# Kernel optimization log

Hardware: AMD Instinct MI355X
Metric: run time of the kernel (lower is better)

Reference implementation:

```python
import jax, jax.numpy as jnp
from jax import lax
import numpy as np

WS = 5  # window_size
H = 6   # hidden_size
IN = 3 * WS  # 15
OUT = 2


def setup_inputs() -> dict:
    key = jax.random.key(0)
    k1, k2, k3, k4, k5 = jax.random.split(key, 5)
    B, T = 8192, 1024
    one_full_traj = jax.random.normal(k1, (B, T, 3), dtype=jnp.float32)
    # nn.Linear-style params: y = x @ W.T + b
    W1 = jax.random.normal(k2, (H, IN), dtype=jnp.float32) * (1.0 / np.sqrt(IN))
    b1 = jax.random.normal(k3, (H,), dtype=jnp.float32) * 0.05
    W2 = jax.random.normal(k4, (OUT, H), dtype=jnp.float32) * (1.0 / np.sqrt(H))
    b2 = jax.random.normal(k5, (OUT,), dtype=jnp.float32) * 0.05
    return {"one_full_traj": one_full_traj, "W1": W1, "b1": b1, "W2": W2, "b2": b2}


def reference(one_full_traj, W1, b1, W2, b2):
    ws = WS
    B, T, _ = one_full_traj.shape

    def mlp(x):  # [B, 3*ws] -> [B, 2]
        return jnp.tanh(x @ W1.T + b1) @ W2.T + b2

    def make_inp(seq):  # [B, ws, 3] -> [B, 3*ws], channel-major per original cat order
        return jnp.transpose(seq, (0, 2, 1)).reshape(B, 3 * ws)

    # step 0
    out = mlp(make_inp(one_full_traj[:, :ws, :]))[:, None, :]  # [B, 1, 2]

    # warm-up loop t = 1 .. ws-1 (small fixed Python loop, matches original indexing)
    for t in range(1, ws):
        n = out.shape[1]  # == t
        tmp = jnp.concatenate(
            [one_full_traj[:, ws + (t - 1):ws + (t - 1) + n, 0:1], out], axis=2
        )  # [B, t, 3]
        seq = jnp.concatenate([one_full_traj[:, t:ws, :], tmp], axis=1)  # [B, ws, 3]
        out = jnp.concatenate([out, mlp(make_inp(seq))[:, None, :]], axis=1)

    # sliding window of the last ws predictions as carry.
    u = one_full_traj[:, :, 0]  # control channel, [B, T]

    def step(win, t):
        uw = lax.dynamic_slice_in_dim(u, t, ws, axis=1)  # [B, ws]
        seq = jnp.concatenate([uw[:, :, None], win], axis=2)  # [B, ws, 3]
        pred = mlp(make_inp(seq))  # [B, 2]
        win = jnp.concatenate([win[:, 1:, :], pred[:, None, :]], axis=1)
        return win, pred

    ts = jnp.arange(ws, T - ws)
    _, preds = lax.scan(step, out, ts)  # preds: [T-2*ws, B, 2]
    return jnp.concatenate([out, jnp.transpose(preds, (1, 0, 2))], axis=1)  # [B, T-ws, 2]
```

## Files before the change

### kernel.cpp

```cpp
#include <hip/hip_runtime.h>
#include <math.h>

#define TLEN  1024
#define NSTEP 1019

template <int CTRL>
__device__ __forceinline__ float dpp_add(float v) {
    union { int i; float f; } in, out;
    in.f = v;
    out.i = __builtin_amdgcn_update_dpp(0, in.i, CTRL, 0xF, 0xF, false);
    return v + out.f;
}
__device__ __forceinline__ float sum8(float v) {
    v = dpp_add<0xB1>(v);
    v = dpp_add<0x4E>(v);
    v = dpp_add<0x141>(v);
    return v;
}

__device__ __forceinline__ float fast_exp2(float z) {
#if __has_builtin(__builtin_amdgcn_exp2f)
    return __builtin_amdgcn_exp2f(z);
#else
    return exp2f(z);
#endif
}

__global__ __launch_bounds__(64) void MLP_or_nextstep_kernel(
    const float* __restrict__ traj,
    const float* __restrict__ W1,
    const float* __restrict__ b1,
    const float* __restrict__ W2,
    const float* __restrict__ b2,
    float* __restrict__ out)
{
    __shared__ float lds_u[TLEN][8];

    const int lane = threadIdx.x;
    const int g    = lane >> 3;
    const int n    = lane & 7;
    const int bstart = blockIdx.x * 8;
    const int b = bstart + g;

    const float* __restrict__ base = traj + (size_t)b * (TLEN * 3);
    float2* outb = (float2*)out + (size_t)b * NSTEP;
    const bool is_store_lane = (n == 0);

    {
        const int s_elem = lane & 7;
        const int s_row  = lane >> 3;
        const float* __restrict__ sbase = traj + (size_t)(bstart + s_elem) * (TLEN * 3);
        for (int j = 0; j < TLEN / 8; ++j) {
            const float* gp = sbase + (size_t)(8 * j + s_row) * 3;
            __builtin_amdgcn_global_load_lds(
                (const __attribute__((address_space(1))) void*)gp,
                (__attribute__((address_space(3))) void*)&lds_u[8 * j][0],
                4, 0, 0);
        }
    }

    const float KK = 2.8853900817779268f;
    const int nr = (n < 6) ? n : 5;
    float w1row[15], b1r;
#pragma unroll
    for (int j = 0; j < 15; ++j) w1row[j] = KK * W1[nr * 15 + j];
    b1r = KK * b1[nr];
    const float w2a_l = (n < 6) ? W2[n]     : 0.0f;
    const float w2b_l = (n < 6) ? W2[6 + n] : 0.0f;
    const float bias_a = (n == 6) ? b2[0] : 0.0f;
    const float bias_b = (n == 7) ? b2[1] : 0.0f;
    const float c1a = -2.0f * w2a_l, c0a = w2a_l + bias_a;
    const float c1b = -2.0f * w2b_l, c0b = w2b_l + bias_b;

    auto mlp = [&](const float* __restrict__ x, float& ya, float& yb) {
        float z0 = w1row[0] * x[0];
        float z1 = w1row[5] * x[5];
        float z2 = fmaf(w1row[10], x[10], b1r);
#pragma unroll
        for (int j = 1; j < 5; ++j) {
            z0 = fmaf(w1row[j],      x[j],      z0);
            z1 = fmaf(w1row[5 + j],  x[5 + j],  z1);
            z2 = fmaf(w1row[10 + j], x[10 + j], z2);
        }
        float z = (z0 + z1) + z2;
        float r = __builtin_amdgcn_rcpf(fast_exp2(z) + 1.0f);
        ya = sum8(fmaf(c1a, r, c0a));
        yb = sum8(fmaf(c1b, r, c0b));
    };

    float uu[12], vv[5], wc[5];
#pragma unroll
    for (int i = 0; i < 12; ++i) uu[i] = base[i * 3];
#pragma unroll
    for (int i = 0; i < 5; ++i) { vv[i] = base[i * 3 + 1]; wc[i] = base[i * 3 + 2]; }

    float pa[5], pb[5];
    {
        float x[15] = {uu[0],uu[1],uu[2],uu[3],uu[4],
                       vv[0],vv[1],vv[2],vv[3],vv[4],
                       wc[0],wc[1],wc[2],wc[3],wc[4]};
        mlp(x, pa[0], pb[0]);
    }
    {
        float x[15] = {uu[1],uu[2],uu[3],uu[4],uu[5],
                       vv[1],vv[2],vv[3],vv[4],pa[0],
                       wc[1],wc[2],wc[3],wc[4],pb[0]};
        mlp(x, pa[1], pb[1]);
    }
    {
        float x[15] = {uu[2],uu[3],uu[4],uu[6],uu[7],
                       vv[2],vv[3],vv[4],pa[0],pa[1],
                       wc[2],wc[3],wc[4],pb[0],pb[1]};
        mlp(x, pa[2], pb[2]);
    }
    {
        float x[15] = {uu[3],uu[4],uu[7],uu[8],uu[9],
                       vv[3],vv[4],pa[0],pa[1],pa[2],
                       wc[3],wc[4],pb[0],pb[1],pb[2]};
        mlp(x, pa[3], pb[3]);
    }
    {
        float x[15] = {uu[4],uu[8],uu[9],uu[10],uu[11],
                       vv[4],pa[0],pa[1],pa[2],pa[3],
                       wc[4],pb[0],pb[1],pb[2],pb[3]};
        mlp(x, pa[4], pb[4]);
    }
    if (is_store_lane) {
#pragma unroll
        for (int i = 0; i < 5; ++i) outb[i] = make_float2(pa[i], pb[i]);
    }

    __syncthreads();

    float aw[5], bw[5];
#pragma unroll
    for (int i = 0; i < 5; ++i) { aw[i] = pa[i]; bw[i] = pb[i]; }

    const float* up  = &lds_u[5][g];
    const float* upn;
    float2* sp = outb + n + 5;
    float unA[9], unB[9];

#pragma unroll
    for (int i = 0; i < 9; ++i) unA[i] = up[8 * i];
    upn = up + 40;

#define LOADN(BUF)                                                           \
    {                                                                        \
        _Pragma("unroll")                                                    \
        for (int i = 0; i < 9; ++i) BUF[i] = upn[8 * i];                     \
        upn += 40;                                                           \
    }

#define STEP(S, UN, J, M)                                                    \
    {                                                                        \
        float z0 = w1row[0] * UN[S];                                         \
        float z1 = w1row[5] * aw[(S) % 5];                                   \
        float z2 = fmaf(w1row[10], bw[(S) % 5], b1r);                        \
        z0 = fmaf(w1row[1], UN[(S) + 1], z0);                                \
        z1 = fmaf(w1row[6], aw[((S) + 1) % 5], z1);                          \
        z2 = fmaf(w1row[11], bw[((S) + 1) % 5], z2);                         \
        z0 = fmaf(w1row[2], UN[(S) + 2], z0);                                \
        z1 = fmaf(w1row[7], aw[((S) + 2) % 5], z1);                          \
        z2 = fmaf(w1row[12], bw[((S) + 2) % 5], z2);                         \
        z0 = fmaf(w1row[3], UN[(S) + 3], z0);                                \
        z1 = fmaf(w1row[8], aw[((S) + 3) % 5], z1);                          \
        z2 = fmaf(w1row[13], bw[((S) + 3) % 5], z2);                         \
        z0 = fmaf(w1row[4], UN[(S) + 4], z0);                                \
        z1 = fmaf(w1row[9], aw[((S) + 4) % 5], z1);                          \
        z2 = fmaf(w1row[14], bw[((S) + 4) % 5], z2);                         \
        float z = (z0 + z1) + z2;                                            \
        float r = __builtin_amdgcn_rcpf(fast_exp2(z) + 1.0f);                \
        float ya = sum8(fmaf(c1a, r, c0a));                                  \
        float yb = sum8(fmaf(c1b, r, c0b));                                  \
        if (n == (J)) { ka##M = ya; kb##M = yb; }                            \
        aw[(S) % 5] = ya; bw[(S) % 5] = yb;                                  \
    }

#define STORE(M) sp[8 * (M)] = make_float2(ka##M, kb##M);

    for (int sb = 0; sb < 25; ++sb) {
        float ka0 = 0, kb0 = 0, ka1 = 0, kb1 = 0, ka2 = 0, kb2 = 0,
              ka3 = 0, kb3 = 0, ka4 = 0, kb4 = 0;
        LOADN(unB)
        STEP(0, unA, 0, 0) STEP(1, unA, 1, 0) STEP(2, unA, 2, 0)
        STEP(3, unA, 3, 0) STEP(4, unA, 4, 0)
        LOADN(unA)
        STEP(0, unB, 5, 0) STEP(1, unB, 6, 0) STEP(2, unB, 7, 0) STORE(0)
        STEP(3, unB, 0, 1) STEP(4, unB, 1, 1)
        LOADN(unB)
        STEP(0, unA, 2, 1) STEP(1, unA, 3, 1) STEP(2, unA, 4, 1)
        STEP(3, unA, 5, 1) STEP(4, unA, 6, 1)
        LOADN(unA)
        STEP(0, unB, 7, 1) STORE(1)
        STEP(1, unB, 0, 2) STEP(2, unB, 1, 2) STEP(3, unB, 2, 2) STEP(4, unB, 3, 2)
        LOADN(unB)
        STEP(0, unA, 4, 2) STEP(1, unA, 5, 2) STEP(2, unA, 6, 2)
        STEP(3, unA, 7, 2) STORE(2)
        STEP(4, unA, 0, 3)
        LOADN(unA)
        STEP(0, unB, 1, 3) STEP(1, unB, 2, 3) STEP(2, unB, 3, 3)
        STEP(3, unB, 4, 3) STEP(4, unB, 5, 3)
        LOADN(unB)
        STEP(0, unA, 6, 3) STEP(1, unA, 7, 3) STORE(3)
        STEP(2, unA, 0, 4) STEP(3, unA, 1, 4) STEP(4, unA, 2, 4)
        LOADN(unA)
        STEP(0, unB, 3, 4) STEP(1, unB, 4, 4) STEP(2, unB, 5, 4)
        STEP(3, unB, 6, 4) STEP(4, unB, 7, 4) STORE(4)

        sp += 40;
    }

    float2* tp = outb + 1005;
#define TSTEP(S, UN, K)                                                      \
    {                                                                        \
        float z0 = w1row[0] * UN[S];                                         \
        float z1 = w1row[5] * aw[(S) % 5];                                   \
        float z2 = fmaf(w1row[10], bw[(S) % 5], b1r);                        \
        z0 = fmaf(w1row[1], UN[(S) + 1], z0);                                \
        z1 = fmaf(w1row[6], aw[((S) + 1) % 5], z1);                          \
        z2 = fmaf(w1row[11], bw[((S) + 1) % 5], z2);                         \
        z0 = fmaf(w1row[2], UN[(S) + 2], z0);                                \
        z1 = fmaf(w1row[7], aw[((S) + 2) % 5], z1);                          \
        z2 = fmaf(w1row[12], bw[((S) + 2) % 5], z2);                         \
        z0 = fmaf(w1row[3], UN[(S) + 3], z0);                                \
        z1 = fmaf(w1row[8], aw[((S) + 3) % 5], z1);                          \
        z2 = fmaf(w1row[13], bw[((S) + 3) % 5], z2);                         \
        z0 = fmaf(w1row[4], UN[(S) + 4], z0);                                \
        z1 = fmaf(w1row[9], aw[((S) + 4) % 5], z1);                          \
        z2 = fmaf(w1row[14], bw[((S) + 4) % 5], z2);                         \
        float z = (z0 + z1) + z2;                                            \
        float r = __builtin_amdgcn_rcpf(fast_exp2(z) + 1.0f);                \
        float ya = sum8(fmaf(c1a, r, c0a));                                  \
        float yb = sum8(fmaf(c1b, r, c0b));                                  \
        if (is_store_lane) tp[K] = make_float2(ya, yb);                      \
        aw[(S) % 5] = ya; bw[(S) % 5] = yb;                                  \
    }

    TSTEP(0, unA, 0) TSTEP(1, unA, 1) TSTEP(2, unA, 2) TSTEP(3, unA, 3) TSTEP(4, unA, 4)
    LOADN(unB)
    TSTEP(0, unB, 5) TSTEP(1, unB, 6) TSTEP(2, unB, 7) TSTEP(3, unB, 8) TSTEP(4, unB, 9)
    LOADN(unA)
    TSTEP(0, unA, 10) TSTEP(1, unA, 11) TSTEP(2, unA, 12) TSTEP(3, unA, 13)

#undef TSTEP
#undef STORE
#undef STEP
#undef LOADN
}

extern "C" void kernel_launch(void* const* d_in, const int* in_sizes, int n_in,
                              void* d_out, int out_size, void* d_ws, size_t ws_size,
                              hipStream_t stream) {
    const float* traj = (const float*)d_in[0];
    const float* W1   = (const float*)d_in[1];
    const float* b1   = (const float*)d_in[2];
    const float* W2   = (const float*)d_in[3];
    const float* b2   = (const float*)d_in[4];
    float* out = (float*)d_out;

    const int grid = 8192 / 8;
    MLP_or_nextstep_kernel<<<grid, 64, 0, stream>>>(traj, W1, b1, W2, b2, out);
}
```

Baseline: 246.7 us.

## Shorten the recurrence critical path by precomputing partial pre-activation sums one step ahead

Splits each step's hidden pre-activation into an input-only part and a window part. The input-only part is computed one block of five steps ahead and held in ping-pong register arrays. The window part, minus the newest prediction, is accumulated during the current step's exp/rcp latency. This leaves only two FMAs, an add, exp, rcp and the DPP reductions on the serial dependency chain between steps. The cost is extra registers, and the u-values are prefetched one block further ahead, so LDS reads go further past the last used element.

```diff
diff --git a/kernel.cpp b/kernel.cpp
--- a/kernel.cpp
+++ b/kernel.cpp
@@ -152,29 +152,59 @@
         upn += 40;                                                           \
     }
 
-#define STEP(S, UN, J, M)                                                    \
+    float duC[5], duD[5];
+#pragma unroll
+    for (int i = 0; i < 5; ++i) {
+        float d = w1row[0] * unA[i];
+        d = fmaf(w1row[1], unA[i + 1], d);
+        d = fmaf(w1row[2], unA[i + 2], d);
+        d = fmaf(w1row[3], unA[i + 3], d);
+        d = fmaf(w1row[4], unA[i + 4], d);
+        duC[i] = d;
+    }
+
+    LOADN(unB)
+
+    float pAc, pBc, pAn, pBn;
+    pAc = w1row[5] * aw[0];
+    pAc = fmaf(w1row[6], aw[1], pAc);
+    pAc = fmaf(w1row[7], aw[2], pAc);
+    pAc = fmaf(w1row[8], aw[3], pAc);
+    pBc = fmaf(w1row[10], bw[0], b1r);
+    pBc = fmaf(w1row[11], bw[1], pBc);
+    pBc = fmaf(w1row[12], bw[2], pBc);
+    pBc = fmaf(w1row[13], bw[3], pBc);
+
+#define STEP(S, DUC, DUN, UN, J, M)                                          \
     {                                                                        \
-        float z0 = w1row[0] * UN[S];                                         \
-        float z1 = w1row[5] * aw[(S) % 5];                                   \
-        float z2 = fmaf(w1row[10], bw[(S) % 5], b1r);                        \
-        z0 = fmaf(w1row[1], UN[(S) + 1], z0);                                \
-        z1 = fmaf(w1row[6], aw[((S) + 1) % 5], z1);                          \
-        z2 = fmaf(w1row[11], bw[((S) + 1) % 5], z2);                         \
-        z0 = fmaf(w1row[2], UN[(S) + 2], z0);                                \
-        z1 = fmaf(w1row[7], aw[((S) + 2) % 5], z1);                          \
-        z2 = fmaf(w1row[12], bw[((S) + 2) % 5], z2);                         \
-        z0 = fmaf(w1row[3], UN[(S) + 3], z0);                                \
-        z1 = fmaf(w1row[8], aw[((S) + 3) % 5], z1);                          \
-        z2 = fmaf(w1row[13], bw[((S) + 3) % 5], z2);                         \
-        z0 = fmaf(w1row[4], UN[(S) + 4], z0);                                \
-        z1 = fmaf(w1row[9], aw[((S) + 4) % 5], z1);                          \
-        z2 = fmaf(w1row[14], bw[((S) + 4) % 5], z2);                         \
-        float z = (z0 + z1) + z2;                                            \
-        float r = __builtin_amdgcn_rcpf(fast_exp2(z) + 1.0f);                \
+        float tA = fmaf(w1row[9],  aw[((S) + 4) % 5], pAc);                  \
+        float tB = fmaf(w1row[14], bw[((S) + 4) % 5], pBc);                  \
+        float z  = (DUC[S] + tA) + tB;                                       \
+        float e  = fast_exp2(z);                                             \
+             \
+        pAn = w1row[5] * aw[((S) + 1) % 5];                                  \
+        pAn = fmaf(w1row[6], aw[((S) + 2) % 5], pAn);                        \
+        pAn = fmaf(w1row[7], aw[((S) + 3) % 5], pAn);                        \
+        pAn = fmaf(w1row[8], aw[((S) + 4) % 5], pAn);                        \
+        pBn = fmaf(w1row[10], bw[((S) + 1) % 5], b1r);                       \
+        pBn = fmaf(w1row[11], bw[((S) + 2) % 5], pBn);                       \
+        pBn = fmaf(w1row[12], bw[((S) + 3) % 5], pBn);                       \
+        pBn = fmaf(w1row[13], bw[((S) + 4) % 5], pBn);                       \
+        {                                                                    \
+            float d = w1row[0] * UN[S];                                      \
+            d = fmaf(w1row[1], UN[(S) + 1], d);                              \
+            d = fmaf(w1row[2], UN[(S) + 2], d);                              \
+            d = fmaf(w1row[3], UN[(S) + 3], d);                              \
+            d = fmaf(w1row[4], UN[(S) + 4], d);                              \
+            DUN[S] = d;                                                      \
+        }                                                                    \
+                                        \
+        float r  = __builtin_amdgcn_rcpf(e + 1.0f);                          \
         float ya = sum8(fmaf(c1a, r, c0a));                                  \
         float yb = sum8(fmaf(c1b, r, c0b));                                  \
         if (n == (J)) { ka##M = ya; kb##M = yb; }                            \
         aw[(S) % 5] = ya; bw[(S) % 5] = yb;                                  \
+        pAc = pAn; pBc = pBn;                                                \
     }
 
 #define STORE(M) sp[8 * (M)] = make_float2(ka##M, kb##M);
@@ -182,31 +212,31 @@
     for (int sb = 0; sb < 25; ++sb) {
         float ka0 = 0, kb0 = 0, ka1 = 0, kb1 = 0, ka2 = 0, kb2 = 0,
               ka3 = 0, kb3 = 0, ka4 = 0, kb4 = 0;
-        LOADN(unB)
-        STEP(0, unA, 0, 0) STEP(1, unA, 1, 0) STEP(2, unA, 2, 0)
-        STEP(3, unA, 3, 0) STEP(4, unA, 4, 0)
-        LOADN(unA)
-        STEP(0, unB, 5, 0) STEP(1, unB, 6, 0) STEP(2, unB, 7, 0) STORE(0)
-        STEP(3, unB, 0, 1) STEP(4, unB, 1, 1)
-        LOADN(unB)
-        STEP(0, unA, 2, 1) STEP(1, unA, 3, 1) STEP(2, unA, 4, 1)
-        STEP(3, unA, 5, 1) STEP(4, unA, 6, 1)
-        LOADN(unA)
-        STEP(0, unB, 7, 1) STORE(1)
-        STEP(1, unB, 0, 2) STEP(2, unB, 1, 2) STEP(3, unB, 2, 2) STEP(4, unB, 3, 2)
-        LOADN(unB)
-        STEP(0, unA, 4, 2) STEP(1, unA, 5, 2) STEP(2, unA, 6, 2)
-        STEP(3, unA, 7, 2) STORE(2)
-        STEP(4, unA, 0, 3)
-        LOADN(unA)
-        STEP(0, unB, 1, 3) STEP(1, unB, 2, 3) STEP(2, unB, 3, 3)
-        STEP(3, unB, 4, 3) STEP(4, unB, 5, 3)
-        LOADN(unB)
-        STEP(0, unA, 6, 3) STEP(1, unA, 7, 3) STORE(3)
-        STEP(2, unA, 0, 4) STEP(3, unA, 1, 4) STEP(4, unA, 2, 4)
-        LOADN(unA)
-        STEP(0, unB, 3, 4) STEP(1, unB, 4, 4) STEP(2, unB, 5, 4)
-        STEP(3, unB, 6, 4) STEP(4, unB, 7, 4) STORE(4)
+        LOADN(unA)
+        STEP(0, duC, duD, unB, 0, 0) STEP(1, duC, duD, unB, 1, 0) STEP(2, duC, duD, unB, 2, 0)
+        STEP(3, duC, duD, unB, 3, 0) STEP(4, duC, duD, unB, 4, 0)
+        LOADN(unB)
+        STEP(0, duD, duC, unA, 5, 0) STEP(1, duD, duC, unA, 6, 0) STEP(2, duD, duC, unA, 7, 0) STORE(0)
+        STEP(3, duD, duC, unA, 0, 1) STEP(4, duD, duC, unA, 1, 1)
+        LOADN(unA)
+        STEP(0, duC, duD, unB, 2, 1) STEP(1, duC, duD, unB, 3, 1) STEP(2, duC, duD, unB, 4, 1)
+        STEP(3, duC, duD, unB, 5, 1) STEP(4, duC, duD, unB, 6, 1)
+        LOADN(unB)
+        STEP(0, duD, duC, unA, 7, 1) STORE(1)
+        STEP(1, duD, duC, unA, 0, 2) STEP(2, duD, duC, unA, 1, 2) STEP(3, duD, duC, unA, 2, 2) STEP(4, duD, duC, unA, 3, 2)
+        LOADN(unA)
+        STEP(0, duC, duD, unB, 4, 2) STEP(1, duC, duD, unB, 5, 2) STEP(2, duC, duD, unB, 6, 2)
+        STEP(3, duC, duD, unB, 7, 2) STORE(2)
+        STEP(4, duC, duD, unB, 0, 3)
+        LOADN(unB)
+        STEP(0, duD, duC, unA, 1, 3) STEP(1, duD, duC, unA, 2, 3) STEP(2, duD, duC, unA, 3, 3)
+        STEP(3, duD, duC, unA, 4, 3) STEP(4, duD, duC, unA, 5, 3)
+        LOADN(unA)
+        STEP(0, duC, duD, unB, 6, 3) STEP(1, duC, duD, unB, 7, 3) STORE(3)
+        STEP(2, duC, duD, unB, 0, 4) STEP(3, duC, duD, unB, 1, 4) STEP(4, duC, duD, unB, 2, 4)
+        LOADN(unB)
+        STEP(0, duD, duC, unA, 3, 4) STEP(1, duD, duC, unA, 4, 4) STEP(2, duD, duC, unA, 5, 4)
+        STEP(3, duD, duC, unA, 6, 4) STEP(4, duD, duC, unA, 7, 4) STORE(4)
 
         sp += 40;
     }
@@ -238,9 +268,8 @@
     }
 
     TSTEP(0, unA, 0) TSTEP(1, unA, 1) TSTEP(2, unA, 2) TSTEP(3, unA, 3) TSTEP(4, unA, 4)
-    LOADN(unB)
+    LOADN(unA)
     TSTEP(0, unB, 5) TSTEP(1, unB, 6) TSTEP(2, unB, 7) TSTEP(3, unB, 8) TSTEP(4, unB, 9)
-    LOADN(unA)
     TSTEP(0, unA, 10) TSTEP(1, unA, 11) TSTEP(2, unA, 12) TSTEP(3, unA, 13)
 
 #undef TSTEP
```

New measurement: 238.7 us. 1.03x faster.

## Interleave two independent trajectories per lane and precompute off-critical-path partial sums

Applied to the files above, without the earlier changes.

Each wave now handles 16 batch rows instead of 8, processing two independent recurrences (X and Y) interleaved per lane so their dependent exp/rcp/DPP chains can hide each other's latency. The control-input contribution and the first four terms of the feedback dot products are precomputed one step ahead, which shortens the serial dependency chain per step. The DPP reductions are batched four at a time. In exchange, register pressure roughly doubles, LDS use doubles, and the grid halves to 512 workgroups, which may underfill the GPU's compute units.

```diff
diff --git a/kernel.cpp b/kernel.cpp
--- a/kernel.cpp
+++ b/kernel.cpp
@@ -16,6 +16,11 @@
     v = dpp_add<0x4E>(v);
     v = dpp_add<0x141>(v);
     return v;
+}
+__device__ __forceinline__ void sum8x4(float& a, float& b, float& c, float& d) {
+    a = dpp_add<0xB1>(a);  b = dpp_add<0xB1>(b);  c = dpp_add<0xB1>(c);  d = dpp_add<0xB1>(d);
+    a = dpp_add<0x4E>(a);  b = dpp_add<0x4E>(b);  c = dpp_add<0x4E>(c);  d = dpp_add<0x4E>(d);
+    a = dpp_add<0x141>(a); b = dpp_add<0x141>(b); c = dpp_add<0x141>(c); d = dpp_add<0x141>(d);
 }
 
 __device__ __forceinline__ float fast_exp2(float z) {
@@ -34,27 +39,30 @@
     const float* __restrict__ b2,
     float* __restrict__ out)
 {
-    __shared__ float lds_u[TLEN][8];
+    __shared__ float lds_u[TLEN][16];
 
     const int lane = threadIdx.x;
     const int g    = lane >> 3;
     const int n    = lane & 7;
-    const int bstart = blockIdx.x * 8;
-    const int b = bstart + g;
-
-    const float* __restrict__ base = traj + (size_t)b * (TLEN * 3);
-    float2* outb = (float2*)out + (size_t)b * NSTEP;
+    const int bstart = blockIdx.x * 16;
+    const int bX = bstart + g;
+    const int bY = bstart + 8 + g;
+
+    const float* __restrict__ baseX = traj + (size_t)bX * (TLEN * 3);
+    const float* __restrict__ baseY = traj + (size_t)bY * (TLEN * 3);
+    float2* outbX = (float2*)out + (size_t)bX * NSTEP;
+    float2* outbY = (float2*)out + (size_t)bY * NSTEP;
     const bool is_store_lane = (n == 0);
 
     {
-        const int s_elem = lane & 7;
-        const int s_row  = lane >> 3;
+        const int s_elem = lane & 15;
+        const int s_row  = lane >> 4;
         const float* __restrict__ sbase = traj + (size_t)(bstart + s_elem) * (TLEN * 3);
-        for (int j = 0; j < TLEN / 8; ++j) {
-            const float* gp = sbase + (size_t)(8 * j + s_row) * 3;
+        for (int j = 0; j < TLEN / 4; ++j) {
+            const float* gp = sbase + (size_t)(4 * j + s_row) * 3;
             __builtin_amdgcn_global_load_lds(
                 (const __attribute__((address_space(1))) void*)gp,
-                (__attribute__((address_space(3))) void*)&lds_u[8 * j][0],
+                (__attribute__((address_space(3))) void*)&lds_u[4 * j][0],
                 4, 0, 0);
         }
     }
@@ -88,165 +96,272 @@
         yb = sum8(fmaf(c1b, r, c0b));
     };
 
-    float uu[12], vv[5], wc[5];
-#pragma unroll
-    for (int i = 0; i < 12; ++i) uu[i] = base[i * 3];
-#pragma unroll
-    for (int i = 0; i < 5; ++i) { vv[i] = base[i * 3 + 1]; wc[i] = base[i * 3 + 2]; }
-
-    float pa[5], pb[5];
-    {
-        float x[15] = {uu[0],uu[1],uu[2],uu[3],uu[4],
-                       vv[0],vv[1],vv[2],vv[3],vv[4],
-                       wc[0],wc[1],wc[2],wc[3],wc[4]};
-        mlp(x, pa[0], pb[0]);
-    }
-    {
-        float x[15] = {uu[1],uu[2],uu[3],uu[4],uu[5],
-                       vv[1],vv[2],vv[3],vv[4],pa[0],
-                       wc[1],wc[2],wc[3],wc[4],pb[0]};
-        mlp(x, pa[1], pb[1]);
-    }
-    {
-        float x[15] = {uu[2],uu[3],uu[4],uu[6],uu[7],
-                       vv[2],vv[3],vv[4],pa[0],pa[1],
-                       wc[2],wc[3],wc[4],pb[0],pb[1]};
-        mlp(x, pa[2], pb[2]);
-    }
-    {
-        float x[15] = {uu[3],uu[4],uu[7],uu[8],uu[9],
-                       vv[3],vv[4],pa[0],pa[1],pa[2],
-                       wc[3],wc[4],pb[0],pb[1],pb[2]};
-        mlp(x, pa[3], pb[3]);
-    }
-    {
-        float x[15] = {uu[4],uu[8],uu[9],uu[10],uu[11],
-                       vv[4],pa[0],pa[1],pa[2],pa[3],
-                       wc[4],pb[0],pb[1],pb[2],pb[3]};
-        mlp(x, pa[4], pb[4]);
-    }
-    if (is_store_lane) {
-#pragma unroll
-        for (int i = 0; i < 5; ++i) outb[i] = make_float2(pa[i], pb[i]);
-    }
+    float paX[5], pbX[5], paY[5], pbY[5];
+
+#define WARMUP(SFX)                                                              \
+    {                                                                            \
+        float uu[12], vv[5], wc[5];                                              \
+        _Pragma("unroll")                                                        \
+        for (int i = 0; i < 12; ++i) uu[i] = base##SFX[i * 3];                   \
+        _Pragma("unroll")                                                        \
+        for (int i = 0; i < 5; ++i) { vv[i] = base##SFX[i * 3 + 1];              \
+                                      wc[i] = base##SFX[i * 3 + 2]; }            \
+        {                                                                        \
+            float x[15] = {uu[0],uu[1],uu[2],uu[3],uu[4],                        \
+                           vv[0],vv[1],vv[2],vv[3],vv[4],                        \
+                           wc[0],wc[1],wc[2],wc[3],wc[4]};                       \
+            mlp(x, pa##SFX[0], pb##SFX[0]);                                      \
+        }                                                                        \
+        {                                                                        \
+            float x[15] = {uu[1],uu[2],uu[3],uu[4],uu[5],                        \
+                           vv[1],vv[2],vv[3],vv[4],pa##SFX[0],                   \
+                           wc[1],wc[2],wc[3],wc[4],pb##SFX[0]};                  \
+            mlp(x, pa##SFX[1], pb##SFX[1]);                                      \
+        }                                                                        \
+        {                                                                        \
+            float x[15] = {uu[2],uu[3],uu[4],uu[6],uu[7],                        \
+                           vv[2],vv[3],vv[4],pa##SFX[0],pa##SFX[1],              \
+                           wc[2],wc[3],wc[4],pb##SFX[0],pb##SFX[1]};             \
+            mlp(x, pa##SFX[2], pb##SFX[2]);                                      \
+        }                                                                        \
+        {                                                                        \
+            float x[15] = {uu[3],uu[4],uu[7],uu[8],uu[9],                        \
+                           vv[3],vv[4],pa##SFX[0],pa##SFX[1],pa##SFX[2],         \
+                           wc[3],wc[4],pb##SFX[0],pb##SFX[1],pb##SFX[2]};        \
+            mlp(x, pa##SFX[3], pb##SFX[3]);                                      \
+        }                                                                        \
+        {                                                                        \
+            float x[15] = {uu[4],uu[8],uu[9],uu[10],uu[11],                      \
+                           vv[4],pa##SFX[0],pa##SFX[1],pa##SFX[2],pa##SFX[3],    \
+                           wc[4],pb##SFX[0],pb##SFX[1],pb##SFX[2],pb##SFX[3]};   \
+            mlp(x, pa##SFX[4], pb##SFX[4]);                                      \
+        }                                                                        \
+        if (is_store_lane) {                                                     \
+            _Pragma("unroll")                                                    \
+            for (int i = 0; i < 5; ++i)                                          \
+                outb##SFX[i] = make_float2(pa##SFX[i], pb##SFX[i]);              \
+        }                                                                        \
+    }
+
+    WARMUP(X)
+    WARMUP(Y)
+#undef WARMUP
 
     __syncthreads();
 
-    float aw[5], bw[5];
-#pragma unroll
-    for (int i = 0; i < 5; ++i) { aw[i] = pa[i]; bw[i] = pb[i]; }
-
-    const float* up  = &lds_u[5][g];
-    const float* upn;
-    float2* sp = outb + n + 5;
-    float unA[9], unB[9];
-
-#pragma unroll
-    for (int i = 0; i < 9; ++i) unA[i] = up[8 * i];
-    upn = up + 40;
-
-#define LOADN(BUF)                                                           \
+    float awX[5], bwX[5], awY[5], bwY[5];
+#pragma unroll
+    for (int i = 0; i < 5; ++i) { awX[i] = paX[i]; bwX[i] = pbX[i];
+                                  awY[i] = paY[i]; bwY[i] = pbY[i]; }
+
+    const float* upX = &lds_u[5][g];
+    const float* upY = &lds_u[5][8 + g];
+    float2* spX = outbX + n + 5;
+    float2* spY = outbY + n + 5;
+    float unAX[9], unBX[9], unAY[9], unBY[9];
+
+#pragma unroll
+    for (int i = 0; i < 9; ++i) { unAX[i] = upX[16 * i]; unAY[i] = upY[16 * i]; }
+    const float* upnX = upX + 80;
+    const float* upnY = upY + 80;
+
+#define LOADN2(UB)                                                           \
     {                                                                        \
         _Pragma("unroll")                                                    \
-        for (int i = 0; i < 9; ++i) BUF[i] = upn[8 * i];                     \
-        upn += 40;                                                           \
-    }
-
-#define STEP(S, UN, J, M)                                                    \
+        for (int i = 0; i < 9; ++i) { un##UB##X[i] = upnX[16 * i];           \
+                                      un##UB##Y[i] = upnY[16 * i]; }         \
+        upnX += 80; upnY += 80;                                              \
+    }
+
+    float duCX[5], duDX[5], duCY[5], duDY[5];
+#pragma unroll
+    for (int i = 0; i < 5; ++i) {
+        float dX = w1row[0] * unAX[i];
+        float dY = w1row[0] * unAY[i];
+        dX = fmaf(w1row[1], unAX[i + 1], dX);
+        dY = fmaf(w1row[1], unAY[i + 1], dY);
+        dX = fmaf(w1row[2], unAX[i + 2], dX);
+        dY = fmaf(w1row[2], unAY[i + 2], dY);
+        dX = fmaf(w1row[3], unAX[i + 3], dX);
+        dY = fmaf(w1row[3], unAY[i + 3], dY);
+        dX = fmaf(w1row[4], unAX[i + 4], dX);
+        dY = fmaf(w1row[4], unAY[i + 4], dY);
+        duCX[i] = dX;
+        duCY[i] = dY;
+    }
+
+    LOADN2(B)
+
+    float pAcX, pBcX, pAnX, pBnX, pAcY, pBcY, pAnY, pBnY;
+    pAcX = w1row[5] * awX[0];
+    pAcY = w1row[5] * awY[0];
+    pAcX = fmaf(w1row[6], awX[1], pAcX);
+    pAcY = fmaf(w1row[6], awY[1], pAcY);
+    pAcX = fmaf(w1row[7], awX[2], pAcX);
+    pAcY = fmaf(w1row[7], awY[2], pAcY);
+    pAcX = fmaf(w1row[8], awX[3], pAcX);
+    pAcY = fmaf(w1row[8], awY[3], pAcY);
+    pBcX = fmaf(w1row[10], bwX[0], b1r);
+    pBcY = fmaf(w1row[10], bwY[0], b1r);
+    pBcX = fmaf(w1row[11], bwX[1], pBcX);
+    pBcY = fmaf(w1row[11], bwY[1], pBcY);
+    pBcX = fmaf(w1row[12], bwX[2], pBcX);
+    pBcY = fmaf(w1row[12], bwY[2], pBcY);
+    pBcX = fmaf(w1row[13], bwX[3], pBcX);
+    pBcY = fmaf(w1row[13], bwY[3], pBcY);
+
+#define STEP2(S, DC, DN, UB, J, M)                                           \
     {                                                                        \
-        float z0 = w1row[0] * UN[S];                                         \
-        float z1 = w1row[5] * aw[(S) % 5];                                   \
-        float z2 = fmaf(w1row[10], bw[(S) % 5], b1r);                        \
-        z0 = fmaf(w1row[1], UN[(S) + 1], z0);                                \
-        z1 = fmaf(w1row[6], aw[((S) + 1) % 5], z1);                          \
-        z2 = fmaf(w1row[11], bw[((S) + 1) % 5], z2);                         \
-        z0 = fmaf(w1row[2], UN[(S) + 2], z0);                                \
-        z1 = fmaf(w1row[7], aw[((S) + 2) % 5], z1);                          \
-        z2 = fmaf(w1row[12], bw[((S) + 2) % 5], z2);                         \
-        z0 = fmaf(w1row[3], UN[(S) + 3], z0);                                \
-        z1 = fmaf(w1row[8], aw[((S) + 3) % 5], z1);                          \
-        z2 = fmaf(w1row[13], bw[((S) + 3) % 5], z2);                         \
-        z0 = fmaf(w1row[4], UN[(S) + 4], z0);                                \
-        z1 = fmaf(w1row[9], aw[((S) + 4) % 5], z1);                          \
-        z2 = fmaf(w1row[14], bw[((S) + 4) % 5], z2);                         \
-        float z = (z0 + z1) + z2;                                            \
-        float r = __builtin_amdgcn_rcpf(fast_exp2(z) + 1.0f);                \
-        float ya = sum8(fmaf(c1a, r, c0a));                                  \
-        float yb = sum8(fmaf(c1b, r, c0b));                                  \
-        if (n == (J)) { ka##M = ya; kb##M = yb; }                            \
-        aw[(S) % 5] = ya; bw[(S) % 5] = yb;                                  \
-    }
-
-#define STORE(M) sp[8 * (M)] = make_float2(ka##M, kb##M);
+        float tAX = fmaf(w1row[9],  awX[((S) + 4) % 5], pAcX);               \
+        float tAY = fmaf(w1row[9],  awY[((S) + 4) % 5], pAcY);               \
+        float tBX = fmaf(w1row[14], bwX[((S) + 4) % 5], pBcX);               \
+        float tBY = fmaf(w1row[14], bwY[((S) + 4) % 5], pBcY);               \
+        float zX  = (du##DC##X[S] + tAX) + tBX;                              \
+        float zY  = (du##DC##Y[S] + tAY) + tBY;                              \
+        float exX = fast_exp2(zX);                                           \
+        float exY = fast_exp2(zY);                                           \
+        pAnX = w1row[5] * awX[((S) + 1) % 5];                                \
+        pAnY = w1row[5] * awY[((S) + 1) % 5];                                \
+        pAnX = fmaf(w1row[6], awX[((S) + 2) % 5], pAnX);                     \
+        pAnY = fmaf(w1row[6], awY[((S) + 2) % 5], pAnY);                     \
+        pAnX = fmaf(w1row[7], awX[((S) + 3) % 5], pAnX);                     \
+        pAnY = fmaf(w1row[7], awY[((S) + 3) % 5], pAnY);                     \
+        pAnX = fmaf(w1row[8], awX[((S) + 4) % 5], pAnX);                     \
+        pAnY = fmaf(w1row[8], awY[((S) + 4) % 5], pAnY);                     \
+        pBnX = fmaf(w1row[10], bwX[((S) + 1) % 5], b1r);                     \
+        pBnY = fmaf(w1row[10], bwY[((S) + 1) % 5], b1r);                     \
+        pBnX = fmaf(w1row[11], bwX[((S) + 2) % 5], pBnX);                    \
+        pBnY = fmaf(w1row[11], bwY[((S) + 2) % 5], pBnY);                    \
+        pBnX = fmaf(w1row[12], bwX[((S) + 3) % 5], pBnX);                    \
+        pBnY = fmaf(w1row[12], bwY[((S) + 3) % 5], pBnY);                    \
+        pBnX = fmaf(w1row[13], bwX[((S) + 4) % 5], pBnX);                    \
+        pBnY = fmaf(w1row[13], bwY[((S) + 4) % 5], pBnY);                    \
+        {                                                                    \
+            float dX = w1row[0] * un##UB##X[S];                              \
+            float dY = w1row[0] * un##UB##Y[S];                              \
+            dX = fmaf(w1row[1], un##UB##X[(S) + 1], dX);                     \
+            dY = fmaf(w1row[1], un##UB##Y[(S) + 1], dY);                     \
+            dX = fmaf(w1row[2], un##UB##X[(S) + 2], dX);                     \
+            dY = fmaf(w1row[2], un##UB##Y[(S) + 2], dY);                     \
+            dX = fmaf(w1row[3], un##UB##X[(S) + 3], dX);                     \
+            dY = fmaf(w1row[3], un##UB##Y[(S) + 3], dY);                     \
+            dX = fmaf(w1row[4], un##UB##X[(S) + 4], dX);                     \
+            dY = fmaf(w1row[4], un##UB##Y[(S) + 4], dY);                     \
+            du##DN##X[S] = dX;                                               \
+            du##DN##Y[S] = dY;                                               \
+        }                                                                    \
+        float rX = __builtin_amdgcn_rcpf(exX + 1.0f);                        \
+        float rY = __builtin_amdgcn_rcpf(exY + 1.0f);                        \
+        float vaX = fmaf(c1a, rX, c0a);                                      \
+        float vbX = fmaf(c1b, rX, c0b);                                      \
+        float vaY = fmaf(c1a, rY, c0a);                                      \
+        float vbY = fmaf(c1b, rY, c0b);                                      \
+        sum8x4(vaX, vbX, vaY, vbY);                                          \
+        if (n == (J)) { kaX##M = vaX; kbX##M = vbX;                          \
+                        kaY##M = vaY; kbY##M = vbY; }                        \
+        awX[(S) % 5] = vaX; bwX[(S) % 5] = vbX;                              \
+        awY[(S) % 5] = vaY; bwY[(S) % 5] = vbY;                              \
+        pAcX = pAnX; pBcX = pBnX; pAcY = pAnY; pBcY = pBnY;                  \
+    }
+
+#define STORE2(M)                                                            \
+    {                                                                        \
+        spX[8 * (M)] = make_float2(kaX##M, kbX##M);                          \
+        spY[8 * (M)] = make_float2(kaY##M, kbY##M);                          \
+    }
 
     for (int sb = 0; sb < 25; ++sb) {
-        float ka0 = 0, kb0 = 0, ka1 = 0, kb1 = 0, ka2 = 0, kb2 = 0,
-              ka3 = 0, kb3 = 0, ka4 = 0, kb4 = 0;
-        LOADN(unB)
-        STEP(0, unA, 0, 0) STEP(1, unA, 1, 0) STEP(2, unA, 2, 0)
-        STEP(3, unA, 3, 0) STEP(4, unA, 4, 0)
-        LOADN(unA)
-        STEP(0, unB, 5, 0) STEP(1, unB, 6, 0) STEP(2, unB, 7, 0) STORE(0)
-        STEP(3, unB, 0, 1) STEP(4, unB, 1, 1)
-        LOADN(unB)
-        STEP(0, unA, 2, 1) STEP(1, unA, 3, 1) STEP(2, unA, 4, 1)
-        STEP(3, unA, 5, 1) STEP(4, unA, 6, 1)
-        LOADN(unA)
-        STEP(0, unB, 7, 1) STORE(1)
-        STEP(1, unB, 0, 2) STEP(2, unB, 1, 2) STEP(3, unB, 2, 2) STEP(4, unB, 3, 2)
-        LOADN(unB)
-        STEP(0, unA, 4, 2) STEP(1, unA, 5, 2) STEP(2, unA, 6, 2)
-        STEP(3, unA, 7, 2) STORE(2)
-        STEP(4, unA, 0, 3)
-        LOADN(unA)
-        STEP(0, unB, 1, 3) STEP(1, unB, 2, 3) STEP(2, unB, 3, 3)
-        STEP(3, unB, 4, 3) STEP(4, unB, 5, 3)
-        LOADN(unB)
-        STEP(0, unA, 6, 3) STEP(1, unA, 7, 3) STORE(3)
-        STEP(2, unA, 0, 4) STEP(3, unA, 1, 4) STEP(4, unA, 2, 4)
-        LOADN(unA)
-        STEP(0, unB, 3, 4) STEP(1, unB, 4, 4) STEP(2, unB, 5, 4)
-        STEP(3, unB, 6, 4) STEP(4, unB, 7, 4) STORE(4)
-
-        sp += 40;
-    }
-
-    float2* tp = outb + 1005;
-#define TSTEP(S, UN, K)                                                      \
+        float kaX0 = 0, kbX0 = 0, kaX1 = 0, kbX1 = 0, kaX2 = 0, kbX2 = 0,
+              kaX3 = 0, kbX3 = 0, kaX4 = 0, kbX4 = 0;
+        float kaY0 = 0, kbY0 = 0, kaY1 = 0, kbY1 = 0, kaY2 = 0, kbY2 = 0,
+              kaY3 = 0, kbY3 = 0, kaY4 = 0, kbY4 = 0;
+        LOADN2(A)
+        STEP2(0, C, D, B, 0, 0) STEP2(1, C, D, B, 1, 0) STEP2(2, C, D, B, 2, 0)
+        STEP2(3, C, D, B, 3, 0) STEP2(4, C, D, B, 4, 0)
+        LOADN2(B)
+        STEP2(0, D, C, A, 5, 0) STEP2(1, D, C, A, 6, 0) STEP2(2, D, C, A, 7, 0) STORE2(0)
+        STEP2(3, D, C, A, 0, 1) STEP2(4, D, C, A, 1, 1)
+        LOADN2(A)
+        STEP2(0, C, D, B, 2, 1) STEP2(1, C, D, B, 3, 1) STEP2(2, C, D, B, 4, 1)
+        STEP2(3, C, D, B, 5, 1) STEP2(4, C, D, B, 6, 1)
+        LOADN2(B)
+        STEP2(0, D, C, A, 7, 1) STORE2(1)
+        STEP2(1, D, C, A, 0, 2) STEP2(2, D, C, A, 1, 2) STEP2(3, D, C, A, 2, 2) STEP2(4, D, C, A, 3, 2)
+        LOADN2(A)
+        STEP2(0, C, D, B, 4, 2) STEP2(1, C, D, B, 5, 2) STEP2(2, C, D, B, 6, 2)
+        STEP2(3, C, D, B, 7, 2) STORE2(2)
+        STEP2(4, C, D, B, 0, 3)
+        LOADN2(B)
+        STEP2(0, D, C, A, 1, 3) STEP2(1, D, C, A, 2, 3) STEP2(2, D, C, A, 3, 3)
+        STEP2(3, D, C, A, 4, 3) STEP2(4, D, C, A, 5, 3)
+        LOADN2(A)
+        STEP2(0, C, D, B, 6, 3) STEP2(1, C, D, B, 7, 3) STORE2(3)
+        STEP2(2, C, D, B, 0, 4) STEP2(3, C, D, B, 1, 4) STEP2(4, C, D, B, 2, 4)
+        LOADN2(B)
+        STEP2(0, D, C, A, 3, 4) STEP2(1, D, C, A, 4, 4) STEP2(2, D, C, A, 5, 4)
+        STEP2(3, D, C, A, 6, 4) STEP2(4, D, C, A, 7, 4) STORE2(4)
+
+        spX += 40; spY += 40;
+    }
+
+    float2* tpX = outbX + 1005;
+    float2* tpY = outbY + 1005;
+#define TSTEP2(S, UB, K)                                                     \
     {                                                                        \
-        float z0 = w1row[0] * UN[S];                                         \
-        float z1 = w1row[5] * aw[(S) % 5];                                   \
-        float z2 = fmaf(w1row[10], bw[(S) % 5], b1r);                        \
-        z0 = fmaf(w1row[1], UN[(S) + 1], z0);                                \
-        z1 = fmaf(w1row[6], aw[((S) + 1) % 5], z1);                          \
-        z2 = fmaf(w1row[11], bw[((S) + 1) % 5], z2);                         \
-        z0 = fmaf(w1row[2], UN[(S) + 2], z0);                                \
-        z1 = fmaf(w1row[7], aw[((S) + 2) % 5], z1);                          \
-        z2 = fmaf(w1row[12], bw[((S) + 2) % 5], z2);                         \
-        z0 = fmaf(w1row[3], UN[(S) + 3], z0);                                \
-        z1 = fmaf(w1row[8], aw[((S) + 3) % 5], z1);                          \
-        z2 = fmaf(w1row[13], bw[((S) + 3) % 5], z2);                         \
-        z0 = fmaf(w1row[4], UN[(S) + 4], z0);                                \
-        z1 = fmaf(w1row[9], aw[((S) + 4) % 5], z1);                          \
-        z2 = fmaf(w1row[14], bw[((S) + 4) % 5], z2);                         \
-        float z = (z0 + z1) + z2;                                            \
-        float r = __builtin_amdgcn_rcpf(fast_exp2(z) + 1.0f);                \
-        float ya = sum8(fmaf(c1a, r, c0a));                                  \
-        float yb = sum8(fmaf(c1b, r, c0b));                                  \
-        if (is_store_lane) tp[K] = make_float2(ya, yb);                      \
-        aw[(S) % 5] = ya; bw[(S) % 5] = yb;                                  \
-    }
-
-    TSTEP(0, unA, 0) TSTEP(1, unA, 1) TSTEP(2, unA, 2) TSTEP(3, unA, 3) TSTEP(4, unA, 4)
-    LOADN(unB)
-    TSTEP(0, unB, 5) TSTEP(1, unB, 6) TSTEP(2, unB, 7) TSTEP(3, unB, 8) TSTEP(4, unB, 9)
-    LOADN(unA)
-    TSTEP(0, unA, 10) TSTEP(1, unA, 11) TSTEP(2, unA, 12) TSTEP(3, unA, 13)
-
-#undef TSTEP
-#undef STORE
-#undef STEP
-#undef LOADN
+        float z0X = w1row[0] * un##UB##X[S];                                 \
+        float z0Y = w1row[0] * un##UB##Y[S];                                 \
+        float z1X = w1row[5] * awX[(S) % 5];                                 \
+        float z1Y = w1row[5] * awY[(S) % 5];                                 \
+        float z2X = fmaf(w1row[10], bwX[(S) % 5], b1r);                      \
+        float z2Y = fmaf(w1row[10], bwY[(S) % 5], b1r);                      \
+        z0X = fmaf(w1row[1], un##UB##X[(S) + 1], z0X);                       \
+        z0Y = fmaf(w1row[1], un##UB##Y[(S) + 1], z0Y);                       \
+        z1X = fmaf(w1row[6], awX[((S) + 1) % 5], z1X);                       \
+        z1Y = fmaf(w1row[6], awY[((S) + 1) % 5], z1Y);                       \
+        z2X = fmaf(w1row[11], bwX[((S) + 1) % 5], z2X);                      \
+        z2Y = fmaf(w1row[11], bwY[((S) + 1) % 5], z2Y);                      \
+        z0X = fmaf(w1row[2], un##UB##X[(S) + 2], z0X);                       \
+        z0Y = fmaf(w1row[2], un##UB##Y[(S) + 2], z0Y);                       \
+        z1X = fmaf(w1row[7], awX[((S) + 2) % 5], z1X);                       \
+        z1Y = fmaf(w1row[7], awY[((S) + 2) % 5], z1Y);                       \
+        z2X = fmaf(w1row[12], bwX[((S) + 2) % 5], z2X);                      \
+        z2Y = fmaf(w1row[12], bwY[((S) + 2) % 5], z2Y);                      \
+        z0X = fmaf(w1row[3], un##UB##X[(S) + 3], z0X);                       \
+        z0Y = fmaf(w1row[3], un##UB##Y[(S) + 3], z0Y);                       \
+        z1X = fmaf(w1row[8], awX[((S) + 3) % 5], z1X);                       \
+        z1Y = fmaf(w1row[8], awY[((S) + 3) % 5], z1Y);                       \
+        z2X = fmaf(w1row[13], bwX[((S) + 3) % 5], z2X);                      \
+        z2Y = fmaf(w1row[13], bwY[((S) + 3) % 5], z2Y);                      \
+        z0X = fmaf(w1row[4], un##UB##X[(S) + 4], z0X);                       \
+        z0Y = fmaf(w1row[4], un##UB##Y[(S) + 4], z0Y);                       \
+        z1X = fmaf(w1row[9], awX[((S) + 4) % 5], z1X);                       \
+        z1Y = fmaf(w1row[9], awY[((S) + 4) % 5], z1Y);                       \
+        z2X = fmaf(w1row[14], bwX[((S) + 4) % 5], z2X);                      \
+        z2Y = fmaf(w1row[14], bwY[((S) + 4) % 5], z2Y);                      \
+        float zX = (z0X + z1X) + z2X;                                        \
+        float zY = (z0Y + z1Y) + z2Y;                                        \
+        float rX = __builtin_amdgcn_rcpf(fast_exp2(zX) + 1.0f);              \
+        float rY = __builtin_amdgcn_rcpf(fast_exp2(zY) + 1.0f);              \
+        float vaX = fmaf(c1a, rX, c0a);                                      \
+        float vbX = fmaf(c1b, rX, c0b);                                      \
+        float vaY = fmaf(c1a, rY, c0a);                                      \
+        float vbY = fmaf(c1b, rY, c0b);                                      \
+        sum8x4(vaX, vbX, vaY, vbY);                                          \
+        if (is_store_lane) { tpX[K] = make_float2(vaX, vbX);                 \
+                             tpY[K] = make_float2(vaY, vbY); }               \
+        awX[(S) % 5] = vaX; bwX[(S) % 5] = vbX;                              \
+        awY[(S) % 5] = vaY; bwY[(S) % 5] = vbY;                              \
+    }
+
+    TSTEP2(0, A, 0) TSTEP2(1, A, 1) TSTEP2(2, A, 2) TSTEP2(3, A, 3) TSTEP2(4, A, 4)
+    LOADN2(A)
+    TSTEP2(0, B, 5) TSTEP2(1, B, 6) TSTEP2(2, B, 7) TSTEP2(3, B, 8) TSTEP2(4, B, 9)
+    TSTEP2(0, A, 10) TSTEP2(1, A, 11) TSTEP2(2, A, 12) TSTEP2(3, A, 13)
+
+#undef TSTEP2
+#undef STORE2
+#undef STEP2
+#undef LOADN2
 }
 
 extern "C" void kernel_launch(void* const* d_in, const int* in_sizes, int n_in,
@@ -259,6 +374,6 @@
     const float* b2   = (const float*)d_in[4];
     float* out = (float*)d_out;
 
-    const int grid = 8192 / 8;
+    const int grid = 8192 / 16;
     MLP_or_nextstep_kernel<<<grid, 64, 0, stream>>>(traj, W1, b1, W2, b2, out);
 }
```

After: 324.0 us. 1.31x slower.
